# Performance work log

Measured on AMD Instinct MI355X. Metric: run time of the kernel, lower is better.

## Reference

```python
import jax, jax.numpy as jnp
import numpy as np

B, T, D, H = 2, 2048, 1024, 16
DK = D // H
NEG = -1e9  # stand-in for -inf; causal mask guarantees >=1 valid key per row


def setup_inputs() -> dict:
    key = jax.random.key(0)
    ks = jax.random.split(key, 9)
    s = 1.0 / np.sqrt(D)
    x = jax.random.normal(ks[0], (B, T, D), dtype=jnp.float32)
    mask = jnp.broadcast_to(jnp.tril(jnp.ones((T, T), dtype=jnp.int32))[None, None], (B, 1, T, T))
    params = {}
    for i, n in enumerate(['q', 'k', 'v', 'o']):
        params['W' + n] = jax.random.normal(ks[1 + 2 * i], (D, D), dtype=jnp.float32) * s
        params['b' + n] = jax.random.normal(ks[2 + 2 * i], (D,), dtype=jnp.float32) * s
    return dict(x=x, mask=mask, **params)


def reference(x, mask, Wq, bq, Wk, bk, Wv, bv, Wo, bo):
    Bx, Tx, Dx = x.shape
    # projections: [B,T,D] -> [B,H,T,DK]
    def split_heads(y):
        return y.reshape(Bx, Tx, H, DK).transpose(0, 2, 1, 3)
    Q = split_heads(x @ Wq + bq)
    K = split_heads(x @ Wk + bk)
    V = split_heads(x @ Wv + bv)
    scores = jnp.einsum('bhqd,bhkd->bhqk', Q, K) / jnp.sqrt(jnp.float32(DK))
    scores = jnp.where(mask == 0, NEG, scores)
    attn = jax.nn.softmax(scores, axis=-1)  # dropout is identity in eval / p=0
    out = jnp.einsum('bhqk,bhkd->bhqd', attn, V)
    out = out.transpose(0, 2, 1, 3).reshape(Bx, Tx, Dx)
    return out @ Wo + bo
```

## Files before the change

### kernel.cpp

```cpp
#include <hip/hip_runtime.h>
#include <hip/hip_bf16.h>

typedef __bf16 bf16;
typedef __attribute__((ext_vector_type(8))) __bf16 bf16x8;
typedef __attribute__((ext_vector_type(4))) __bf16 bf16x4;
typedef __attribute__((ext_vector_type(4))) float f32x4;

#define TSEQ 2048
#define DMODEL 1024
#define NHEAD 16
#define DKH 64
#define BATCH 2
#define NQKV 3072
#define PSTR 72

typedef __attribute__((address_space(1))) const void gv_t;
typedef __attribute__((address_space(3))) void sv_t;
__device__ __forceinline__ void gll16(const bf16* g, bf16* s) {
    __builtin_amdgcn_global_load_lds((gv_t*)g, (sv_t*)s, 16, 0, 0);
}
__device__ __forceinline__ void wait_vm0() {
    __builtin_amdgcn_s_waitcnt(0x0F70);
}

__global__ __launch_bounds__(256) void convert_bf16(
    const float* __restrict__ in, bf16* __restrict__ out)
{
    int i = (blockIdx.x * 256 + threadIdx.x) * 4;
    f32x4 v = *(const f32x4*)(in + i);
    bf16x4 o;
#pragma unroll
    for (int j = 0; j < 4; ++j) o[j] = (bf16)v[j];
    *(bf16x4*)(out + i) = o;
}

__global__ __launch_bounds__(256) void bias_concat(
    const float* __restrict__ bq, const float* __restrict__ bk,
    const float* __restrict__ bv, float* __restrict__ out)
{
    int i = blockIdx.x * 256 + threadIdx.x;
    float v = i < 1024 ? bq[i] : i < 2048 ? bk[i - 1024] : bv[i - 2048];
    out[i] = v;
}

__global__ __launch_bounds__(256) void transpose_w(
    const float* __restrict__ W0, const float* __restrict__ W1,
    const float* __restrict__ W2, const float* __restrict__ W3,
    bf16* __restrict__ WT)
{
    __shared__ float t[32][33];
    const float* W = blockIdx.z == 0 ? W0 : blockIdx.z == 1 ? W1
                   : blockIdx.z == 2 ? W2 : W3;
    bf16* T = WT + (size_t)blockIdx.z * DMODEL * DMODEL;
    int bx = blockIdx.x * 32, by = blockIdx.y * 32;
    int tx = threadIdx.x, ty = threadIdx.y;
#pragma unroll
    for (int i = 0; i < 4; ++i)
        t[ty + i * 8][tx] = W[(size_t)(by + ty + i * 8) * DMODEL + bx + tx];
    __syncthreads();
#pragma unroll
    for (int i = 0; i < 4; ++i)
        T[(size_t)(bx + ty + i * 8) * DMODEL + by + tx] = (bf16)t[tx][ty + i * 8];
}

__global__ __launch_bounds__(256) void transpose_v(
    const bf16* __restrict__ QKV, bf16* __restrict__ VT)
{
    __shared__ bf16 t[32][33];
    int b = blockIdx.z >> 4, h = blockIdx.z & 15;
    int t0 = blockIdx.x * 32, d0 = blockIdx.y * 32;
    int tx = threadIdx.x, ty = threadIdx.y;
#pragma unroll
    for (int i = 0; i < 4; ++i)
        t[ty + i * 8][tx] =
            QKV[(size_t)(b * TSEQ + t0 + ty + i * 8) * NQKV + 2048 + h * DKH + d0 + tx];
    __syncthreads();
#pragma unroll
    for (int i = 0; i < 4; ++i)
        VT[((size_t)(b * NHEAD + h) * DKH + d0 + ty + i * 8) * TSEQ + t0 + tx] =
            t[tx][ty + i * 8];
}

template <typename OutT>
__global__ __launch_bounds__(256) void gemm_bias_kernel(
    const bf16* __restrict__ A, const bf16* __restrict__ BT,
    const float* __restrict__ bias, OutT* __restrict__ C, int ldc)
{
    __shared__ bf16 As[128 * 32];
    __shared__ bf16 Bs[128 * 32];
    const int tid = threadIdx.x;
    const int ln = tid & 63, wave = tid >> 6;
    const int wm = wave >> 1, wn = wave & 1;
    const int lr = ln & 15, quad = ln >> 4;
    const int m0 = blockIdx.y * 128, n0 = blockIdx.x * 128;

    f32x4 acc[4][4] = {};

    const int grow = wave * 32 + (ln >> 2);
    const int gcol = (ln & 3) * 8;
    const bf16* Ag = A + (size_t)(m0 + grow) * DMODEL + gcol;
    const bf16* Bg = BT + (size_t)(n0 + grow) * DMODEL + gcol;
    bf16* AsW = As + wave * 1024;
    bf16* BsW = Bs + wave * 1024;

    for (int kt = 0; kt < DMODEL / 32; ++kt) {
        const int kk = kt * 32;
#pragma unroll
        for (int l = 0; l < 2; ++l) {
            gll16(Ag + (size_t)(l * 16) * DMODEL + kk, AsW + l * 512);
            gll16(Bg + (size_t)(l * 16) * DMODEL + kk, BsW + l * 512);
        }
        wait_vm0();
        __syncthreads();
        bf16x8 af[4], bfr[4];
#pragma unroll
        for (int i = 0; i < 4; ++i)
            af[i] = *(const bf16x8*)(As + (wm * 64 + i * 16 + lr) * 32 + quad * 8);
#pragma unroll
        for (int j = 0; j < 4; ++j)
            bfr[j] = *(const bf16x8*)(Bs + (wn * 64 + j * 16 + lr) * 32 + quad * 8);
#pragma unroll
        for (int i = 0; i < 4; ++i)
#pragma unroll
            for (int j = 0; j < 4; ++j)
                acc[i][j] = __builtin_amdgcn_mfma_f32_16x16x32_bf16(
                    af[i], bfr[j], acc[i][j], 0, 0, 0);
        __syncthreads();
    }

#pragma unroll
    for (int j = 0; j < 4; ++j) {
        int n = n0 + wn * 64 + j * 16 + lr;
        float bv = bias[n];
#pragma unroll
        for (int i = 0; i < 4; ++i) {
            int mb = m0 + wm * 64 + i * 16 + quad * 4;
#pragma unroll
            for (int r = 0; r < 4; ++r)
                C[(size_t)(mb + r) * ldc + n] = (OutT)(acc[i][j][r] + bv);
        }
    }
}

template <bool MASK>
__device__ __forceinline__ void attn_chunk(
    int kc, int q0w, int lr, int quad,
    const bf16* __restrict__ KsB, const bf16* __restrict__ VsB,
    bf16* __restrict__ Pw,
    const bf16x8 qb[2], f32x4 oacc[4], float& lrow)
{
    const int sw = lr & 7;
    bf16x8 kb[4][2];
#pragma unroll
    for (int kt = 0; kt < 4; ++kt)
#pragma unroll
        for (int kk = 0; kk < 2; ++kk)
            kb[kt][kk] = *(const bf16x8*)(KsB + (kt * 16 + lr) * 64 +
                                          (((kk * 4 + quad) ^ sw) * 8));
    f32x4 st[4] = {};
#pragma unroll
    for (int kt = 0; kt < 4; ++kt)
#pragma unroll
        for (int kk = 0; kk < 2; ++kk)
            st[kt] = __builtin_amdgcn_mfma_f32_16x16x32_bf16(
                kb[kt][kk], qb[kk], st[kt], 0, 0, 0);

    const float scale2 = 0.18033688f;
    const int q = q0w + lr;
    float rs = 0.f;
#pragma unroll
    for (int kt = 0; kt < 4; ++kt) {
        bf16x4 p4;
#pragma unroll
        for (int r = 0; r < 4; ++r) {
            float p = exp2f(fmaf(st[kt][r], scale2, -24.0f));
            if (MASK && (kc + kt * 16 + quad * 4 + r > q)) p = 0.f;
            rs += p;
            p4[r] = (bf16)p;
        }
        *(bf16x4*)(Pw + lr * PSTR + kt * 16 + quad * 4) = p4;
    }
    rs += __shfl_xor(rs, 16);
    rs += __shfl_xor(rs, 32);
    lrow += rs;

#pragma unroll
    for (int kk = 0; kk < 2; ++kk) {
        bf16x8 pa = *(const bf16x8*)(Pw + lr * PSTR + kk * 32 + quad * 8);
#pragma unroll
        for (int dt = 0; dt < 4; ++dt) {
            bf16x8 vb = *(const bf16x8*)(VsB + (dt * 16 + lr) * 64 +
                                         (((kk * 4 + quad) ^ sw) * 8));
            oacc[dt] = __builtin_amdgcn_mfma_f32_16x16x32_bf16(
                pa, vb, oacc[dt], 0, 0, 0);
        }
    }
}

__global__ __launch_bounds__(512) void flash_attn(
    const bf16* __restrict__ QKV, const bf16* __restrict__ VT,
    bf16* __restrict__ O)
{
    __shared__ bf16 Ks[2][64 * 64];
    __shared__ bf16 Vs[2][64 * 64];
    __shared__ bf16 Pl[8][16 * PSTR];
    const int tid = threadIdx.x;
    const int ln = tid & 63, w = tid >> 6;
    const int lr = ln & 15, quad = ln >> 4;
    const int h = blockIdx.y, b = blockIdx.z;

    int xb = blockIdx.x;
    if ((h ^ b) & 1) xb = (TSEQ / 128 - 1) - xb;
    const int q0 = xb * 128;
    const int q0w = q0 + w * 16;
    bf16* Pw = Pl[w];

    const bf16* Qb = QKV + (size_t)b * TSEQ * NQKV + h * DKH;
    const bf16* Kb = Qb + 1024;
    const bf16* VTb = VT + (size_t)(b * NHEAD + h) * DKH * TSEQ;

    const int srow = (w & 3) * 16 + (ln >> 3);
    const int scol = ((ln & 7) ^ ((ln >> 3) & 7)) * 8;
    const bool stK = (w < 4);

    auto stage = [&](int buf, int kc) {
        if (stK) {
            const bf16* g = Kb + (size_t)(kc + srow) * NQKV + scol;
            bf16* s = &Ks[buf][(w & 3) * 16 * 64];
#pragma unroll
            for (int l = 0; l < 2; ++l)
                gll16(g + (size_t)(l * 8) * NQKV, s + l * 8 * 64);
        } else {
            const bf16* g = VTb + (size_t)srow * TSEQ + kc + scol;
            bf16* s = &Vs[buf][(w & 3) * 16 * 64];
#pragma unroll
            for (int l = 0; l < 2; ++l)
                gll16(g + (size_t)(l * 8) * TSEQ, s + l * 8 * 64);
        }
    };

    bf16x8 qb[2];
#pragma unroll
    for (int kk = 0; kk < 2; ++kk)
        qb[kk] = *(const bf16x8*)(Qb + (size_t)(q0w + lr) * NQKV +
                                  kk * 32 + quad * 8);

    f32x4 oacc[4] = {};
    float lrow = 0.f;

    const int nch = (q0 + 128) >> 6;
    stage(0, 0);
    wait_vm0();
    __syncthreads();
    for (int c = 0; c < nch; ++c) {
        if (c + 1 < nch) stage((c + 1) & 1, (c + 1) * 64);
        const int kc = c * 64;
        if (kc <= q0w + 15) {
            if (kc + 63 <= q0w)
                attn_chunk<false>(kc, q0w, lr, quad, Ks[c & 1], Vs[c & 1], Pw,
                                  qb, oacc, lrow);
            else
                attn_chunk<true>(kc, q0w, lr, quad, Ks[c & 1], Vs[c & 1], Pw,
                                 qb, oacc, lrow);
        }
        wait_vm0();
        __syncthreads();
    }

#pragma unroll
    for (int r = 0; r < 4; ++r) {
        float inv = 1.0f / __shfl(lrow, quad * 4 + r);
        int row = q0w + quad * 4 + r;
#pragma unroll
        for (int dt = 0; dt < 4; ++dt)
            O[(size_t)(b * TSEQ + row) * DMODEL + h * DKH + dt * 16 + lr] =
                (bf16)(oacc[dt][r] * inv);
    }
}

extern "C" void kernel_launch(void* const* d_in, const int* in_sizes, int n_in,
                              void* d_out, int out_size, void* d_ws, size_t ws_size,
                              hipStream_t stream)
{
    const float* x  = (const float*)d_in[0];
    const float* Wq = (const float*)d_in[2];
    const float* bq = (const float*)d_in[3];
    const float* Wk = (const float*)d_in[4];
    const float* bk = (const float*)d_in[5];
    const float* Wv = (const float*)d_in[6];
    const float* bv = (const float*)d_in[7];
    const float* Wo = (const float*)d_in[8];
    const float* bo = (const float*)d_in[9];

    char* ws = (char*)d_ws;
    bf16* xb   = (bf16*)(ws);
    bf16* QKV  = (bf16*)(ws + (8u  << 20));
    bf16* VT   = (bf16*)(ws + (32u << 20));
    bf16* O    = (bf16*)(ws + (40u << 20));
    bf16* WT   = (bf16*)(ws + (48u << 20));
    float* wsBias = (float*)VT;

    const int NX = BATCH * TSEQ * DMODEL;
    convert_bf16<<<NX / (256 * 4), 256, 0, stream>>>(x, xb);

    dim3 tb(32, 8);
    transpose_w<<<dim3(32, 32, 4), tb, 0, stream>>>(Wq, Wk, Wv, Wo, WT);
    bias_concat<<<NQKV / 256, 256, 0, stream>>>(bq, bk, bv, wsBias);

    gemm_bias_kernel<bf16><<<dim3(NQKV / 128, 32), 256, 0, stream>>>(
        xb, WT, wsBias, QKV, NQKV);

    transpose_v<<<dim3(TSEQ / 32, DKH / 32, BATCH * NHEAD), tb, 0, stream>>>(QKV, VT);

    flash_attn<<<dim3(TSEQ / 128, NHEAD, BATCH), 512, 0, stream>>>(QKV, VT, O);

    gemm_bias_kernel<float><<<dim3(DMODEL / 128, 32), 256, 0, stream>>>(
        O, WT + 3u * (1u << 20), bo, (float*)d_out, DMODEL);
}
```

Measured before the change: 217.5 us.

## Fuse prologue kernels, write V transposed from GEMM, swizzle LDS, split-K output GEMM

Merges the x conversion, weight transposes and bias concat into one prologue launch. The QKV GEMM epilogue now writes V directly in transposed layout, which removes the separate transpose_v kernel. GEMM LDS tiles get an XOR swizzle to reduce bank conflicts. The output projection is split-K into two partials, and a reduce kernel then adds the partials and the bias. This trades an extra fp32 round trip for more blocks in the output GEMM.

```diff
diff --git a/kernel.cpp b/kernel.cpp
--- a/kernel.cpp
+++ b/kernel.cpp
@@ -23,68 +23,47 @@
     __builtin_amdgcn_s_waitcnt(0x0F70);
 }
 
-__global__ __launch_bounds__(256) void convert_bf16(
-    const float* __restrict__ in, bf16* __restrict__ out)
-{
-    int i = (blockIdx.x * 256 + threadIdx.x) * 4;
-    f32x4 v = *(const f32x4*)(in + i);
-    bf16x4 o;
-#pragma unroll
-    for (int j = 0; j < 4; ++j) o[j] = (bf16)v[j];
-    *(bf16x4*)(out + i) = o;
-}
-
-__global__ __launch_bounds__(256) void bias_concat(
-    const float* __restrict__ bq, const float* __restrict__ bk,
-    const float* __restrict__ bv, float* __restrict__ out)
-{
-    int i = blockIdx.x * 256 + threadIdx.x;
-    float v = i < 1024 ? bq[i] : i < 2048 ? bk[i - 1024] : bv[i - 2048];
-    out[i] = v;
-}
-
-__global__ __launch_bounds__(256) void transpose_w(
+__global__ __launch_bounds__(256) void prologue(
+    const float* __restrict__ x,
     const float* __restrict__ W0, const float* __restrict__ W1,
     const float* __restrict__ W2, const float* __restrict__ W3,
-    bf16* __restrict__ WT)
+    const float* __restrict__ bq, const float* __restrict__ bk,
+    const float* __restrict__ bv,
+    bf16* __restrict__ xb, bf16* __restrict__ WT, float* __restrict__ wsBias)
 {
     __shared__ float t[32][33];
-    const float* W = blockIdx.z == 0 ? W0 : blockIdx.z == 1 ? W1
-                   : blockIdx.z == 2 ? W2 : W3;
-    bf16* T = WT + (size_t)blockIdx.z * DMODEL * DMODEL;
-    int bx = blockIdx.x * 32, by = blockIdx.y * 32;
-    int tx = threadIdx.x, ty = threadIdx.y;
-#pragma unroll
-    for (int i = 0; i < 4; ++i)
-        t[ty + i * 8][tx] = W[(size_t)(by + ty + i * 8) * DMODEL + bx + tx];
-    __syncthreads();
-#pragma unroll
-    for (int i = 0; i < 4; ++i)
-        T[(size_t)(bx + ty + i * 8) * DMODEL + by + tx] = (bf16)t[tx][ty + i * 8];
-}
-
-__global__ __launch_bounds__(256) void transpose_v(
-    const bf16* __restrict__ QKV, bf16* __restrict__ VT)
-{
-    __shared__ bf16 t[32][33];
-    int b = blockIdx.z >> 4, h = blockIdx.z & 15;
-    int t0 = blockIdx.x * 32, d0 = blockIdx.y * 32;
-    int tx = threadIdx.x, ty = threadIdx.y;
-#pragma unroll
-    for (int i = 0; i < 4; ++i)
-        t[ty + i * 8][tx] =
-            QKV[(size_t)(b * TSEQ + t0 + ty + i * 8) * NQKV + 2048 + h * DKH + d0 + tx];
-    __syncthreads();
-#pragma unroll
-    for (int i = 0; i < 4; ++i)
-        VT[((size_t)(b * NHEAD + h) * DKH + d0 + ty + i * 8) * TSEQ + t0 + tx] =
-            t[tx][ty + i * 8];
+    const int bid = blockIdx.x, tid = threadIdx.x;
+    if (bid < 4096) {
+        const int mz = bid >> 10, tt = bid & 1023;
+        const float* W = mz == 0 ? W0 : mz == 1 ? W1 : mz == 2 ? W2 : W3;
+        bf16* T = WT + (size_t)mz * DMODEL * DMODEL;
+        const int bx = (tt & 31) * 32, by = (tt >> 5) * 32;
+        const int tx = tid & 31, ty = tid >> 5;
+#pragma unroll
+        for (int i = 0; i < 4; ++i)
+            t[ty + i * 8][tx] = W[(size_t)(by + ty + i * 8) * DMODEL + bx + tx];
+        __syncthreads();
+#pragma unroll
+        for (int i = 0; i < 4; ++i)
+            T[(size_t)(bx + ty + i * 8) * DMODEL + by + tx] = (bf16)t[tx][ty + i * 8];
+    } else if (bid < 8192) {
+        int i = ((bid - 4096) * 256 + tid) * 4;
+        f32x4 v = *(const f32x4*)(x + i);
+        bf16x4 o;
+#pragma unroll
+        for (int j = 0; j < 4; ++j) o[j] = (bf16)v[j];
+        *(bf16x4*)(xb + i) = o;
+    } else {
+        int i = (bid - 8192) * 256 + tid;
+        wsBias[i] = i < 1024 ? bq[i] : i < 2048 ? bk[i - 1024] : bv[i - 2048];
+    }
 }
 
 template <typename OutT>
 __global__ __launch_bounds__(256) void gemm_bias_kernel(
     const bf16* __restrict__ A, const bf16* __restrict__ BT,
-    const float* __restrict__ bias, OutT* __restrict__ C, int ldc)
+    const float* __restrict__ bias, OutT* __restrict__ C0,
+    OutT* __restrict__ C1, int ldc, bf16* __restrict__ Vout, int ksteps)
 {
     __shared__ bf16 As[128 * 32];
     __shared__ bf16 Bs[128 * 32];
@@ -93,32 +72,36 @@
     const int wm = wave >> 1, wn = wave & 1;
     const int lr = ln & 15, quad = ln >> 4;
     const int m0 = blockIdx.y * 128, n0 = blockIdx.x * 128;
+    const int k0 = blockIdx.z * ksteps * 32;
+    OutT* C = blockIdx.z == 0 ? C0 : C1;
 
     f32x4 acc[4][4] = {};
 
     const int grow = wave * 32 + (ln >> 2);
-    const int gcol = (ln & 3) * 8;
-    const bf16* Ag = A + (size_t)(m0 + grow) * DMODEL + gcol;
-    const bf16* Bg = BT + (size_t)(n0 + grow) * DMODEL + gcol;
+    const int gch = (ln & 3) ^ ((ln >> 2) & 3);
+    const bf16* Ag = A + (size_t)(m0 + grow) * DMODEL + gch * 8;
+    const bf16* Bg = BT + (size_t)(n0 + grow) * DMODEL + gch * 8;
     bf16* AsW = As + wave * 1024;
     bf16* BsW = Bs + wave * 1024;
-
-    for (int kt = 0; kt < DMODEL / 32; ++kt) {
-        const int kk = kt * 32;
-#pragma unroll
-        for (int l = 0; l < 2; ++l) {
-            gll16(Ag + (size_t)(l * 16) * DMODEL + kk, AsW + l * 512);
-            gll16(Bg + (size_t)(l * 16) * DMODEL + kk, BsW + l * 512);
-        }
+    const int rsw = (lr & 3);
+
+    for (int kt = 0; kt < ksteps; ++kt) {
+        const int kk = k0 + kt * 32;
+        gll16(Ag + kk, AsW);
+        gll16(Ag + (size_t)16 * DMODEL + kk, AsW + 512);
+        gll16(Bg + kk, BsW);
+        gll16(Bg + (size_t)16 * DMODEL + kk, BsW + 512);
         wait_vm0();
         __syncthreads();
         bf16x8 af[4], bfr[4];
 #pragma unroll
         for (int i = 0; i < 4; ++i)
-            af[i] = *(const bf16x8*)(As + (wm * 64 + i * 16 + lr) * 32 + quad * 8);
+            af[i] = *(const bf16x8*)(As + (wm * 64 + i * 16 + lr) * 32 +
+                                     ((quad ^ rsw) * 8));
 #pragma unroll
         for (int j = 0; j < 4; ++j)
-            bfr[j] = *(const bf16x8*)(Bs + (wn * 64 + j * 16 + lr) * 32 + quad * 8);
+            bfr[j] = *(const bf16x8*)(Bs + (wn * 64 + j * 16 + lr) * 32 +
+                                      ((quad ^ rsw) * 8));
 #pragma unroll
         for (int i = 0; i < 4; ++i)
 #pragma unroll
@@ -128,18 +111,50 @@
         __syncthreads();
     }
 
-#pragma unroll
-    for (int j = 0; j < 4; ++j) {
-        int n = n0 + wn * 64 + j * 16 + lr;
-        float bv = bias[n];
-#pragma unroll
-        for (int i = 0; i < 4; ++i) {
-            int mb = m0 + wm * 64 + i * 16 + quad * 4;
-#pragma unroll
-            for (int r = 0; r < 4; ++r)
-                C[(size_t)(mb + r) * ldc + n] = (OutT)(acc[i][j][r] + bv);
-        }
-    }
+    if (Vout != nullptr && n0 >= 2048) {
+        const int bb = m0 >> 11;
+        const int tb_ = (m0 & (TSEQ - 1)) + wm * 64;
+#pragma unroll
+        for (int j = 0; j < 4; ++j) {
+            int n = n0 + wn * 64 + j * 16 + lr;
+            int hd = n - 2048;
+            float bv = bias[n];
+            bf16* vrow = Vout + ((size_t)(bb * DMODEL + hd)) * TSEQ;
+#pragma unroll
+            for (int i = 0; i < 4; ++i) {
+                int t = tb_ + i * 16 + quad * 4;
+                bf16x4 v4;
+#pragma unroll
+                for (int r = 0; r < 4; ++r) v4[r] = (bf16)(acc[i][j][r] + bv);
+                *(bf16x4*)(vrow + t) = v4;
+            }
+        }
+    } else {
+#pragma unroll
+        for (int j = 0; j < 4; ++j) {
+            int n = n0 + wn * 64 + j * 16 + lr;
+            float bv = bias ? bias[n] : 0.f;
+#pragma unroll
+            for (int i = 0; i < 4; ++i) {
+                int mb = m0 + wm * 64 + i * 16 + quad * 4;
+#pragma unroll
+                for (int r = 0; r < 4; ++r)
+                    C[(size_t)(mb + r) * ldc + n] = (OutT)(acc[i][j][r] + bv);
+            }
+        }
+    }
+}
+
+__global__ __launch_bounds__(256) void reduce_out(
+    const float* __restrict__ P1, const float* __restrict__ bias,
+    float* __restrict__ out)
+{
+    int i = (blockIdx.x * 256 + threadIdx.x) * 4;
+    f32x4 a = *(const f32x4*)(out + i);
+    f32x4 b = *(const f32x4*)(P1 + i);
+    f32x4 bi = *(const f32x4*)(bias + (i & (DMODEL - 1)));
+    f32x4 r = a + b + bi;
+    *(f32x4*)(out + i) = r;
 }
 
 template <bool MASK>
@@ -298,22 +313,21 @@
     bf16* VT   = (bf16*)(ws + (32u << 20));
     bf16* O    = (bf16*)(ws + (40u << 20));
     bf16* WT   = (bf16*)(ws + (48u << 20));
-    float* wsBias = (float*)VT;
-
-    const int NX = BATCH * TSEQ * DMODEL;
-    convert_bf16<<<NX / (256 * 4), 256, 0, stream>>>(x, xb);
-
-    dim3 tb(32, 8);
-    transpose_w<<<dim3(32, 32, 4), tb, 0, stream>>>(Wq, Wk, Wv, Wo, WT);
-    bias_concat<<<NQKV / 256, 256, 0, stream>>>(bq, bk, bv, wsBias);
-
-    gemm_bias_kernel<bf16><<<dim3(NQKV / 128, 32), 256, 0, stream>>>(
-        xb, WT, wsBias, QKV, NQKV);
-
-    transpose_v<<<dim3(TSEQ / 32, DKH / 32, BATCH * NHEAD), tb, 0, stream>>>(QKV, VT);
+    float* wsBias = (float*)O;
+    float* P1  = (float*)QKV;
+
+    prologue<<<8204, 256, 0, stream>>>(x, Wq, Wk, Wv, Wo, bq, bk, bv,
+                                       xb, WT, wsBias);
+
+    gemm_bias_kernel<bf16><<<dim3(NQKV / 128, 32, 1), 256, 0, stream>>>(
+        xb, WT, wsBias, QKV, QKV, NQKV, VT, DMODEL / 32);
 
     flash_attn<<<dim3(TSEQ / 128, NHEAD, BATCH), 512, 0, stream>>>(QKV, VT, O);
 
-    gemm_bias_kernel<float><<<dim3(DMODEL / 128, 32), 256, 0, stream>>>(
-        O, WT + 3u * (1u << 20), bo, (float*)d_out, DMODEL);
-}
+    gemm_bias_kernel<float><<<dim3(DMODEL / 128, 32, 2), 256, 0, stream>>>(
+        O, WT + 3u * (1u << 20), nullptr, (float*)d_out, P1, DMODEL, nullptr,
+        DMODEL / 64);
+
+    reduce_out<<<(BATCH * TSEQ * DMODEL) / 1024, 256, 0, stream>>>(
+        P1, bo, (float*)d_out);
+}
```

New measurement: 232.9 us. 1.07x slower.
